# Kernel tuning notes

Hardware: AMD Instinct MI355X
Metric: run time of the kernel (lower is better)

The kernel has to match this reference:

```python
import jax, jax.numpy as jnp
import numpy as np
import math

N_HEAD = 16


def setup_inputs() -> dict:
    key = jax.random.key(0)
    ks = jax.random.split(key, 5)
    B, T, C = 2, 2048, 2048
    x = jax.random.normal(ks[0], (B, T, C), dtype=jnp.float32)
    # additive causal mask: 0 on/below diagonal, large negative above
    causal = jnp.tril(jnp.ones((T, T), dtype=bool))
    attention_mask = jnp.where(causal, 0.0, -1e9).astype(jnp.float32)[None, None]
    scale = 0.02
    W_attn = jax.random.normal(ks[1], (C, 3 * C), dtype=jnp.float32) * scale
    b_attn = jax.random.normal(ks[2], (3 * C,), dtype=jnp.float32) * scale
    W_proj = jax.random.normal(ks[3], (C, C), dtype=jnp.float32) * scale
    b_proj = jax.random.normal(ks[4], (C,), dtype=jnp.float32) * scale
    return {"x": x, "attention_mask": attention_mask, "W_attn": W_attn,
            "b_attn": b_attn, "W_proj": W_proj, "b_proj": b_proj}


def reference(x, attention_mask, W_attn, b_attn, W_proj, b_proj):
    B, T, C = x.shape
    H = N_HEAD
    Dh = C // H
    qkv = x @ W_attn + b_attn                      # [B,T,3C]
    q, k, v = jnp.split(qkv, 3, axis=2)            # each [B,T,C]
    current_cache = jnp.concatenate([k, v], axis=2)  # [B,T,2C]
    qh = q.reshape(B, T, H, Dh).transpose(0, 2, 1, 3)  # [B,H,T,Dh]
    kh = k.reshape(B, T, H, Dh).transpose(0, 2, 1, 3)
    vh = v.reshape(B, T, H, Dh).transpose(0, 2, 1, 3)
    att = jnp.einsum('bhqd,bhkd->bhqk', qh, kh) * (1.0 / math.sqrt(Dh))
    att = att + attention_mask                     # broadcast [1,1,T,T]
    att = jax.nn.softmax(att, axis=-1)
    y = jnp.einsum('bhqk,bhkd->bhqd', att, vh)     # [B,H,T,Dh]
    y = y.transpose(0, 2, 1, 3).reshape(B, T, C)
    y = y @ W_proj + b_proj                        # [B,T,C]
    return (y, current_cache)
```

## Files before the change

### kernel.cpp

```cpp
#include <hip/hip_runtime.h>

typedef __attribute__((ext_vector_type(8))) short bf16x8;
typedef __attribute__((ext_vector_type(4))) float f32x4;

#define MFMA16(a, b, c) __builtin_amdgcn_mfma_f32_16x16x32_bf16((a), (b), (c), 0, 0, 0)

static __device__ __forceinline__ short f2bf(float f) {
  unsigned u = __builtin_bit_cast(unsigned, f);
  unsigned r = (u + 0x7FFFu + ((u >> 16) & 1u)) >> 16;
  return (short)(unsigned short)r;
}
static __device__ __forceinline__ unsigned pack2(float lo, float hi) {
  return (unsigned)(unsigned short)f2bf(lo) | ((unsigned)(unsigned short)f2bf(hi) << 16);
}

static __device__ __forceinline__ void glds16(const void* g, void* l) {
  __builtin_amdgcn_global_load_lds((const __attribute__((address_space(1))) unsigned*)g,
                                   (__attribute__((address_space(3))) unsigned*)l, 16, 0, 0);
}

__global__ __launch_bounds__(256) void cvt_bf16_kernel(const float* __restrict__ in,
                                                       short* __restrict__ out) {
  size_t i = ((size_t)blockIdx.x * 256 + threadIdx.x) * 8;
  float4 a = *(const float4*)(in + i);
  float4 b = *(const float4*)(in + i + 4);
  uint4 o;
  o.x = pack2(a.x, a.y);
  o.y = pack2(a.z, a.w);
  o.z = pack2(b.x, b.y);
  o.w = pack2(b.z, b.w);
  *(uint4*)(out + i) = o;
}

__global__ __launch_bounds__(256) void transpose_cvt_kernel(const float* __restrict__ in,
                                                            short* __restrict__ out, int R,
                                                            int Cc) {
  __shared__ float tile[64][65];
  int tx = threadIdx.x & 15, ty = threadIdx.x >> 4;
  int r0 = blockIdx.y * 64, c0 = blockIdx.x * 64;
#pragma unroll
  for (int i = 0; i < 4; i++) {
    int r = ty + i * 16;
    float4 v = *(const float4*)(in + (size_t)(r0 + r) * Cc + c0 + tx * 4);
    tile[r][tx * 4 + 0] = v.x;
    tile[r][tx * 4 + 1] = v.y;
    tile[r][tx * 4 + 2] = v.z;
    tile[r][tx * 4 + 3] = v.w;
  }
  __syncthreads();
#pragma unroll
  for (int i = 0; i < 4; i++) {
    int co = ty + i * 16;
    uint2 o;
    o.x = pack2(tile[tx * 4 + 0][co], tile[tx * 4 + 1][co]);
    o.y = pack2(tile[tx * 4 + 2][co], tile[tx * 4 + 3][co]);
    *(uint2*)(out + (size_t)(c0 + co) * R + r0 + tx * 4) = o;
  }
}

__global__ __launch_bounds__(256) void gemm_qkv_kernel(const short* __restrict__ A,
                                                       const short* __restrict__ Bt,
                                                       const float* __restrict__ bias,
                                                       short* __restrict__ q_bf,
                                                       short* __restrict__ k_bf,
                                                       short* __restrict__ v_bf,
                                                       float* __restrict__ cache) {
  const int K = 2048;
  __shared__ __align__(16) short smem[128 * 64];
  short* As = smem;
  short* Bs = smem + 128 * 32;
  int tid = threadIdx.x;
  int lane = tid & 63, wid = tid >> 6;
  int wr = wid >> 1, wc = wid & 1;
  int l15 = lane & 15, l4 = lane >> 4;
  int rowBase = blockIdx.y * 128, colBase = blockIdx.x * 128;

  int srow = lane >> 2;
  int schunk = ((lane & 3) ^ ((lane >> 3) & 3)) * 8;
  int g0 = wid * 16, g1 = 64 + wid * 16;
  const short* Ag0 = A + (size_t)(rowBase + g0 + srow) * K + schunk;
  const short* Ag1 = A + (size_t)(rowBase + g1 + srow) * K + schunk;
  const short* Bg0 = Bt + (size_t)(colBase + g0 + srow) * K + schunk;
  const short* Bg1 = Bt + (size_t)(colBase + g1 + srow) * K + schunk;
  short* la0 = &As[g0 * 32];
  short* la1 = &As[g1 * 32];
  short* lb0 = &Bs[g0 * 32];
  short* lb1 = &Bs[g1 * 32];

  int fchunk = (l4 ^ ((l15 >> 1) & 3)) * 8;

  f32x4 zero = {0.f, 0.f, 0.f, 0.f};
  f32x4 acc[4][4];
#pragma unroll
  for (int i = 0; i < 4; i++)
#pragma unroll
    for (int j = 0; j < 4; j++) acc[i][j] = zero;

  for (int k0 = 0; k0 < K; k0 += 32) {
    __syncthreads();
    glds16(Ag0 + k0, la0);
    glds16(Ag1 + k0, la1);
    glds16(Bg0 + k0, lb0);
    glds16(Bg1 + k0, lb1);
    __syncthreads();
    bf16x8 af[4], bfv[4];
#pragma unroll
    for (int mt = 0; mt < 4; mt++)
      af[mt] = *(const bf16x8*)&As[(wr * 64 + mt * 16 + l15) * 32 + fchunk];
#pragma unroll
    for (int nt = 0; nt < 4; nt++)
      bfv[nt] = *(const bf16x8*)&Bs[(wc * 64 + nt * 16 + l15) * 32 + fchunk];
#pragma unroll
    for (int mt = 0; mt < 4; mt++)
#pragma unroll
      for (int nt = 0; nt < 4; nt++) acc[mt][nt] = MFMA16(af[mt], bfv[nt], acc[mt][nt]);
  }

  int seg = colBase >> 11;
  int colLoc = colBase & 2047;
  float scale = (seg == 0) ? 0.08838834764831845f : 1.0f;
  short* outp = (seg == 0) ? q_bf : (seg == 1) ? k_bf : v_bf;
  short(*Cs)[64] = (short(*)[64])smem;

  float bv[4];
#pragma unroll
  for (int nt = 0; nt < 4; nt++) bv[nt] = bias[colBase + wc * 64 + nt * 16 + l15];

#pragma unroll
  for (int p = 0; p < 2; p++) {
    __syncthreads();
    if (wc == p) {
#pragma unroll
      for (int mt = 0; mt < 4; mt++)
#pragma unroll
        for (int nt = 0; nt < 4; nt++)
#pragma unroll
          for (int r = 0; r < 4; r++)
            Cs[wr * 64 + mt * 16 + l4 * 4 + r][nt * 16 + l15] =
                f2bf((acc[mt][nt][r] + bv[nt]) * scale);
    }
    __syncthreads();
#pragma unroll
    for (int q = 0; q < 4; q++) {
      int row = q * 32 + (tid >> 3);
      int c8 = (tid & 7) * 8;
      *(uint4*)(outp + (size_t)(rowBase + row) * 2048 + colLoc + p * 64 + c8) =
          *(const uint4*)&Cs[row][c8];
    }
  }

  if (seg) {
    int coff = (seg == 1) ? 0 : 2048;
#pragma unroll
    for (int mt = 0; mt < 4; mt++)
#pragma unroll
      for (int nt = 0; nt < 4; nt++) {
        int cc = coff + colLoc + wc * 64 + nt * 16 + l15;
#pragma unroll
        for (int r = 0; r < 4; r++) {
          int row = rowBase + wr * 64 + mt * 16 + l4 * 4 + r;
          cache[(size_t)row * 4096 + cc] = acc[mt][nt][r] + bv[nt];
        }
      }
  }
}

__global__ __launch_bounds__(256) void vpost_kernel(const short* __restrict__ vb,
                                                    short* __restrict__ vt) {
  __shared__ short tile[64][72];
  int tid = threadIdx.x;
  int z = blockIdx.z;
  int b = z >> 4, hh = z & 15;
  int t0 = blockIdx.x * 64, d0 = blockIdx.y * 64;
  int tx = tid & 7, ty = tid >> 3;
#pragma unroll
  for (int i = 0; i < 2; i++) {
    int r = ty + i * 32;
    *(uint4*)&tile[r][tx * 8] =
        *(const uint4*)(vb + (size_t)(b * 2048 + t0 + r) * 2048 + hh * 128 + d0 + tx * 8);
  }
  __syncthreads();
#pragma unroll
  for (int i = 0; i < 2; i++) {
    int dr = ty + i * 32;
    short tmp[8];
#pragma unroll
    for (int j = 0; j < 8; j++) {
      int p = tx * 8 + j;
      int tl = (p & 32) + ((p & 1) << 4) + ((p >> 1) & 15);
      tmp[j] = tile[tl][dr];
    }
    *(uint4*)(vt + (size_t)(z * 128 + d0 + dr) * 2048 + t0 + tx * 8) = *(uint4*)tmp;
  }
}

__global__ __launch_bounds__(256) void gemm_proj_kernel(const short* __restrict__ A,
                                                        const short* __restrict__ Bt,
                                                        const float* __restrict__ bias,
                                                        float* __restrict__ out_y) {
  const int K = 2048;
  __shared__ __align__(16) short As[128 * 32];
  __shared__ __align__(16) short Bs[128 * 32];
  int tid = threadIdx.x;
  int lane = tid & 63, wid = tid >> 6;
  int wr = wid >> 1, wc = wid & 1;
  int l15 = lane & 15, l4 = lane >> 4;
  int rowBase = blockIdx.y * 128, colBase = blockIdx.x * 128;

  int srow = lane >> 2;
  int schunk = ((lane & 3) ^ ((lane >> 3) & 3)) * 8;
  int g0 = wid * 16, g1 = 64 + wid * 16;
  const short* Ag0 = A + (size_t)(rowBase + g0 + srow) * K + schunk;
  const short* Ag1 = A + (size_t)(rowBase + g1 + srow) * K + schunk;
  const short* Bg0 = Bt + (size_t)(colBase + g0 + srow) * K + schunk;
  const short* Bg1 = Bt + (size_t)(colBase + g1 + srow) * K + schunk;
  short* la0 = &As[g0 * 32];
  short* la1 = &As[g1 * 32];
  short* lb0 = &Bs[g0 * 32];
  short* lb1 = &Bs[g1 * 32];

  int fchunk = (l4 ^ ((l15 >> 1) & 3)) * 8;

  f32x4 zero = {0.f, 0.f, 0.f, 0.f};
  f32x4 acc[4][4];
#pragma unroll
  for (int i = 0; i < 4; i++)
#pragma unroll
    for (int j = 0; j < 4; j++) acc[i][j] = zero;

  for (int k0 = 0; k0 < K; k0 += 32) {
    __syncthreads();
    glds16(Ag0 + k0, la0);
    glds16(Ag1 + k0, la1);
    glds16(Bg0 + k0, lb0);
    glds16(Bg1 + k0, lb1);
    __syncthreads();
    bf16x8 af[4], bfv[4];
#pragma unroll
    for (int mt = 0; mt < 4; mt++)
      af[mt] = *(const bf16x8*)&As[(wr * 64 + mt * 16 + l15) * 32 + fchunk];
#pragma unroll
    for (int nt = 0; nt < 4; nt++)
      bfv[nt] = *(const bf16x8*)&Bs[(wc * 64 + nt * 16 + l15) * 32 + fchunk];
#pragma unroll
    for (int mt = 0; mt < 4; mt++)
#pragma unroll
      for (int nt = 0; nt < 4; nt++) acc[mt][nt] = MFMA16(af[mt], bfv[nt], acc[mt][nt]);
  }

#pragma unroll
  for (int mt = 0; mt < 4; mt++) {
#pragma unroll
    for (int nt = 0; nt < 4; nt++) {
      int col = colBase + wc * 64 + nt * 16 + l15;
      float bvv = bias[col];
#pragma unroll
      for (int r = 0; r < 4; r++) {
        int row = rowBase + wr * 64 + mt * 16 + l4 * 4 + r;
        out_y[(size_t)row * 2048 + col] = acc[mt][nt][r] + bvv;
      }
    }
  }
}

#define LDK 136
#define LDV 72
#define LDP 72

__global__ __launch_bounds__(512, 4) void attn_kernel(const short* __restrict__ qb,
                                                      const short* __restrict__ kb,
                                                      const short* __restrict__ vtb,
                                                      short* __restrict__ attout) {
  __shared__ short Ks[64 * LDK];
  __shared__ short Vs[128 * LDV];
  __shared__ short Ps[8][16 * LDP];

  int tid = threadIdx.x;
  int lane = tid & 63, wid = tid >> 6;
  int l15 = lane & 15, l4 = lane >> 4;
  int qlo = blockIdx.x, qhi = 31 - qlo;
  int h = blockIdx.y, b = blockIdx.z;
  int myqt = (wid < 4) ? qhi : qlo;
  int qrow0 = myqt * 64 + (wid & 3) * 16;
  size_t qkbase = (size_t)b * 2048 * 2048 + (size_t)h * 128;
  size_t vbase = (size_t)((b * 16 + h) * 128) * 2048;

  bf16x8 qf[4];
#pragma unroll
  for (int kk = 0; kk < 4; kk++)
    qf[kk] = *(const bf16x8*)(qb + qkbase + (size_t)(qrow0 + l15) * 2048 + kk * 32 + l4 * 8);

  short onev = (short)0x3F80;
  bf16x8 ones = {onev, onev, onev, onev, onev, onev, onev, onev};

  f32x4 zero = {0.f, 0.f, 0.f, 0.f};
  f32x4 o[8], ol;
#pragma unroll
  for (int n = 0; n < 8; n++) o[n] = zero;
  ol = zero;

  for (int kt = 0; kt <= qhi; kt++) {
    int kt0 = kt * 64;
    __syncthreads();
#pragma unroll
    for (int i = 0; i < 2; i++) {
      int c = i * 512 + tid;
      int kr = c >> 4, kc = (c & 15) * 8;
      *(uint4*)&Ks[kr * LDK + kc] = *(const uint4*)(kb + qkbase + (size_t)(kt0 + kr) * 2048 + kc);
    }
#pragma unroll
    for (int i = 0; i < 2; i++) {
      int c = i * 512 + tid;
      int dr = c >> 3, tc = (c & 7) * 8;
      *(uint4*)&Vs[dr * LDV + tc] = *(const uint4*)(vtb + vbase + (size_t)dr * 2048 + kt0 + tc);
    }
    __syncthreads();

    if (wid < 4 || kt <= qlo) {
      f32x4 s[4];
#pragma unroll
      for (int nt = 0; nt < 4; nt++) s[nt] = zero;
#pragma unroll
      for (int kk = 0; kk < 4; kk++) {
#pragma unroll
        for (int nt = 0; nt < 4; nt++) {
          bf16x8 kf = *(const bf16x8*)&Ks[(nt * 16 + l15) * LDK + kk * 32 + l4 * 8];
          s[nt] = MFMA16(qf[kk], kf, s[nt]);
        }
      }

      if (kt == myqt) {
#pragma unroll
        for (int nt = 0; nt < 4; nt++) {
          int colg = kt0 + nt * 16 + l15;
#pragma unroll
          for (int r = 0; r < 4; r++) {
            int rowg = qrow0 + l4 * 4 + r;
            if (colg > rowg) s[nt][r] = -1e30f;
          }
        }
      }

#pragma unroll
      for (int r = 0; r < 4; r++) {
        float p0 = __expf(s[0][r]);
        float p1 = __expf(s[1][r]);
        float p2 = __expf(s[2][r]);
        float p3 = __expf(s[3][r]);
        int prow = (l4 * 4 + r) * LDP;
        *(unsigned*)&Ps[wid][prow + 2 * l15] = pack2(p0, p1);
        *(unsigned*)&Ps[wid][prow + 32 + 2 * l15] = pack2(p2, p3);
      }

#pragma unroll
      for (int kk = 0; kk < 2; kk++) {
        bf16x8 pf = *(const bf16x8*)&Ps[wid][l15 * LDP + kk * 32 + l4 * 8];
        ol = MFMA16(pf, ones, ol);
#pragma unroll
        for (int n = 0; n < 8; n++) {
          bf16x8 vf = *(const bf16x8*)&Vs[(n * 16 + l15) * LDV + kk * 32 + l4 * 8];
          o[n] = MFMA16(pf, vf, o[n]);
        }
      }
    }
  }

  float rl[4];
#pragma unroll
  for (int r = 0; r < 4; r++) rl[r] = 1.0f / ol[r];
#pragma unroll
  for (int n = 0; n < 8; n++)
#pragma unroll
    for (int r = 0; r < 4; r++)
      attout[qkbase + (size_t)(qrow0 + l4 * 4 + r) * 2048 + n * 16 + l15] =
          f2bf(o[n][r] * rl[r]);
}

extern "C" void kernel_launch(void* const* d_in, const int* in_sizes, int n_in, void* d_out,
                              int out_size, void* d_ws, size_t ws_size, hipStream_t stream) {
  const float* x = (const float*)d_in[0];
  const float* W_attn = (const float*)d_in[2];
  const float* b_attn = (const float*)d_in[3];
  const float* W_proj = (const float*)d_in[4];
  const float* b_proj = (const float*)d_in[5];
  float* y = (float*)d_out;
  float* cache = y + (size_t)4096 * 2048;

  char* p = (char*)d_ws;
  short* x_bf = (short*)p;   p += (size_t)8388608 * 2;
  short* q_bf = (short*)p;   p += (size_t)8388608 * 2;
  short* k_bf = (short*)p;   p += (size_t)8388608 * 2;
  short* vt_bf = (short*)p;  p += (size_t)8388608 * 2;
  short* att_bf = (short*)p; p += (size_t)8388608 * 2;
  short* wt_attn = (short*)p; p += (size_t)12582912 * 2;
  short* wt_proj = (short*)p; p += (size_t)4194304 * 2;
  short* v_bf = att_bf;

  cvt_bf16_kernel<<<4096, 256, 0, stream>>>(x, x_bf);
  transpose_cvt_kernel<<<dim3(96, 32), 256, 0, stream>>>(W_attn, wt_attn, 2048, 6144);
  transpose_cvt_kernel<<<dim3(32, 32), 256, 0, stream>>>(W_proj, wt_proj, 2048, 2048);
  gemm_qkv_kernel<<<dim3(48, 32), 256, 0, stream>>>(x_bf, wt_attn, b_attn, q_bf, k_bf, v_bf,
                                                    cache);
  vpost_kernel<<<dim3(32, 2, 32), 256, 0, stream>>>(v_bf, vt_bf);
  attn_kernel<<<dim3(16, 16, 2), 512, 0, stream>>>(q_bf, k_bf, vt_bf, att_bf);
  gemm_proj_kernel<<<dim3(16, 32), 256, 0, stream>>>(att_bf, wt_proj, b_proj, y);
}
```

Before: 460.2 us.

## Rewrite QKV GEMM as 256x256 tiles with double-buffered LDS pipelining

```diff
diff --git a/kernel.cpp b/kernel.cpp
--- a/kernel.cpp
+++ b/kernel.cpp
@@ -58,93 +58,170 @@
   }
 }
 
-__global__ __launch_bounds__(256) void gemm_qkv_kernel(const short* __restrict__ A,
-                                                       const short* __restrict__ Bt,
-                                                       const float* __restrict__ bias,
-                                                       short* __restrict__ q_bf,
-                                                       short* __restrict__ k_bf,
-                                                       short* __restrict__ v_bf,
-                                                       float* __restrict__ cache) {
-  const int K = 2048;
-  __shared__ __align__(16) short smem[128 * 64];
-  short* As = smem;
-  short* Bs = smem + 128 * 32;
+
+#define AF(C, KS, MT) (*(const bf16x8*)&lds[(C)*32768 + (KS)*8192 + (wr8 + (MT)) * 512 + rdoff])
+#define BF_(C, KS, NT) \
+  (*(const bf16x8*)&lds[(C)*32768 + 16384 + (KS)*8192 + (wc4 + (NT)) * 512 + rdoff])
+
+#define STAGE_A(C, KS, KT)                                                      \
+  do {                                                                          \
+    glds16(Asrc0 + (KT) * 64 + (KS) * 32, &lds[(C)*32768 + (KS)*8192 + wid * 512]); \
+    glds16(Asrc1 + (KT) * 64 + (KS) * 32,                                       \
+           &lds[(C)*32768 + (KS)*8192 + (wid + 8) * 512]);                      \
+  } while (0)
+#define STAGE_B(C, KS, KT)                                                      \
+  do {                                                                          \
+    glds16(Bsrc0 + (KT) * 64 + (KS) * 32,                                       \
+           &lds[(C)*32768 + 16384 + (KS)*8192 + wid * 512]);                    \
+    glds16(Bsrc1 + (KT) * 64 + (KS) * 32,                                       \
+           &lds[(C)*32768 + 16384 + (KS)*8192 + (wid + 8) * 512]);              \
+  } while (0)
+
+#define MIDBAR                                                       \
+  do {                                                               \
+    asm volatile("s_barrier\n\ts_waitcnt lgkmcnt(0)" ::: "memory");  \
+    __builtin_amdgcn_sched_barrier(0);                               \
+  } while (0)
+#define ENDBAR                                       \
+  do {                                               \
+    __builtin_amdgcn_sched_barrier(0);               \
+    asm volatile("s_barrier" ::: "memory");          \
+    __builtin_amdgcn_sched_barrier(0);               \
+  } while (0)
+#define ENDBARV                                                      \
+  do {                                                               \
+    __builtin_amdgcn_sched_barrier(0);                               \
+    asm volatile("s_waitcnt vmcnt(8)\n\ts_barrier" ::: "memory");    \
+    __builtin_amdgcn_sched_barrier(0);                               \
+  } while (0)
+
+#define MMROW(AR, MT)                          \
+  do {                                         \
+    acc[MT][0] = MFMA16(AR, bfr[0], acc[MT][0]); \
+    acc[MT][1] = MFMA16(AR, bfr[1], acc[MT][1]); \
+    acc[MT][2] = MFMA16(AR, bfr[2], acc[MT][2]); \
+    acc[MT][3] = MFMA16(AR, bfr[3], acc[MT][3]); \
+  } while (0)
+
+#define PHASE(C, KS, MB, STG, WAITV)                                         \
+  do {                                                                       \
+    af[0] = AF(C, KS, MB + 0);                                               \
+    af[1] = AF(C, KS, MB + 1);                                               \
+    af[2] = AF(C, KS, MB + 2);                                               \
+    af[3] = AF(C, KS, MB + 3);                                               \
+    if ((MB) == 0) {                                                         \
+      bfr[0] = BF_(C, KS, 0);                                                \
+      bfr[1] = BF_(C, KS, 1);                                                \
+      bfr[2] = BF_(C, KS, 2);                                                \
+      bfr[3] = BF_(C, KS, 3);                                                \
+    }                                                                        \
+    STG;                                                                     \
+    MIDBAR;                                                                  \
+    __builtin_amdgcn_s_setprio(1);                                           \
+    MMROW(af[0], MB + 0);                                                    \
+    MMROW(af[1], MB + 1);                                                    \
+    MMROW(af[2], MB + 2);                                                    \
+    MMROW(af[3], MB + 3);                                                    \
+    __builtin_amdgcn_s_setprio(0);                                           \
+    if (WAITV) { ENDBARV; } else { ENDBAR; }                                 \
+  } while (0)
+
+#define KTILE(C, NX, MM)                       \
+  do {                                         \
+    int s23 = (MM) + 1 > 31 ? 31 : (MM) + 1;   \
+    int s01 = (MM) + 2 > 31 ? 31 : (MM) + 2;   \
+    PHASE(C, 0, 0, STAGE_A(NX, 1, s23), 0);    \
+    PHASE(C, 0, 4, STAGE_B(NX, 1, s23), 1);    \
+    PHASE(C, 1, 0, STAGE_A(C, 0, s01), 0);     \
+    PHASE(C, 1, 4, STAGE_B(C, 0, s01), 1);     \
+  } while (0)
+
+__global__ __launch_bounds__(512, 2) void gemm_qkv_kernel(const short* __restrict__ A,
+                                                          const short* __restrict__ Bt,
+                                                          const float* __restrict__ bias,
+                                                          short* __restrict__ q_bf,
+                                                          short* __restrict__ k_bf,
+                                                          short* __restrict__ v_bf,
+                                                          float* __restrict__ cache) {
+  __shared__ __align__(16) short lds[65536];
   int tid = threadIdx.x;
   int lane = tid & 63, wid = tid >> 6;
-  int wr = wid >> 1, wc = wid & 1;
   int l15 = lane & 15, l4 = lane >> 4;
-  int rowBase = blockIdx.y * 128, colBase = blockIdx.x * 128;
-
-  int srow = lane >> 2;
-  int schunk = ((lane & 3) ^ ((lane >> 3) & 3)) * 8;
-  int g0 = wid * 16, g1 = 64 + wid * 16;
-  const short* Ag0 = A + (size_t)(rowBase + g0 + srow) * K + schunk;
-  const short* Ag1 = A + (size_t)(rowBase + g1 + srow) * K + schunk;
-  const short* Bg0 = Bt + (size_t)(colBase + g0 + srow) * K + schunk;
-  const short* Bg1 = Bt + (size_t)(colBase + g1 + srow) * K + schunk;
-  short* la0 = &As[g0 * 32];
-  short* la1 = &As[g1 * 32];
-  short* lb0 = &Bs[g0 * 32];
-  short* lb1 = &Bs[g1 * 32];
-
-  int fchunk = (l4 ^ ((l15 >> 1) & 3)) * 8;
+  int wr = wid >> 2, wc = wid & 3;
+  int wr8 = wr * 8, wc4 = wc * 4;
+
+  int bid = blockIdx.x;
+  int s = (bid & 7) * 48 + (bid >> 3);
+  int bx = s % 24, by = s / 24;
+  int rowBase = by * 256, colBase = bx * 256;
+
+  int wprime = (lane * 16) ^ (lane & 32);
+  int r_ = wprime >> 6;
+  int cs_ = (wprime & 63) >> 1;
+  const short* Asrc0 = A + (size_t)(rowBase + wid * 16 + r_) * 2048 + cs_;
+  const short* Asrc1 = A + (size_t)(rowBase + (wid + 8) * 16 + r_) * 2048 + cs_;
+  const short* Bsrc0 = Bt + (size_t)(colBase + wid * 16 + r_) * 2048 + cs_;
+  const short* Bsrc1 = Bt + (size_t)(colBase + (wid + 8) * 16 + r_) * 2048 + cs_;
+
+  int rdoff = l15 * 32 + ((l4 * 8) ^ ((l15 & 8) << 1));
 
   f32x4 zero = {0.f, 0.f, 0.f, 0.f};
-  f32x4 acc[4][4];
-#pragma unroll
-  for (int i = 0; i < 4; i++)
+  f32x4 acc[8][4];
+#pragma unroll
+  for (int i = 0; i < 8; i++)
 #pragma unroll
     for (int j = 0; j < 4; j++) acc[i][j] = zero;
 
-  for (int k0 = 0; k0 < K; k0 += 32) {
-    __syncthreads();
-    glds16(Ag0 + k0, la0);
-    glds16(Ag1 + k0, la1);
-    glds16(Bg0 + k0, lb0);
-    glds16(Bg1 + k0, lb1);
-    __syncthreads();
-    bf16x8 af[4], bfv[4];
-#pragma unroll
-    for (int mt = 0; mt < 4; mt++)
-      af[mt] = *(const bf16x8*)&As[(wr * 64 + mt * 16 + l15) * 32 + fchunk];
-#pragma unroll
-    for (int nt = 0; nt < 4; nt++)
-      bfv[nt] = *(const bf16x8*)&Bs[(wc * 64 + nt * 16 + l15) * 32 + fchunk];
-#pragma unroll
-    for (int mt = 0; mt < 4; mt++)
-#pragma unroll
-      for (int nt = 0; nt < 4; nt++) acc[mt][nt] = MFMA16(af[mt], bfv[nt], acc[mt][nt]);
-  }
+  bf16x8 af[4], bfr[4];
+
+  STAGE_A(0, 0, 0);
+  STAGE_B(0, 0, 0);
+  STAGE_A(0, 1, 0);
+  STAGE_B(0, 1, 0);
+  STAGE_A(1, 0, 1);
+  STAGE_B(1, 0, 1);
+  asm volatile("s_waitcnt vmcnt(8)" ::: "memory");
+  __builtin_amdgcn_sched_barrier(0);
+  asm volatile("s_barrier" ::: "memory");
+  __builtin_amdgcn_sched_barrier(0);
+
+  for (int it = 0; it < 16; ++it) {
+    int m0 = it * 2;
+    KTILE(0, 1, m0);
+    KTILE(1, 0, m0 + 1);
+  }
+
+  asm volatile("s_waitcnt vmcnt(0)" ::: "memory");
+  __syncthreads();
 
   int seg = colBase >> 11;
   int colLoc = colBase & 2047;
   float scale = (seg == 0) ? 0.08838834764831845f : 1.0f;
   short* outp = (seg == 0) ? q_bf : (seg == 1) ? k_bf : v_bf;
-  short(*Cs)[64] = (short(*)[64])smem;
-
   float bv[4];
 #pragma unroll
   for (int nt = 0; nt < 4; nt++) bv[nt] = bias[colBase + wc * 64 + nt * 16 + l15];
 
-#pragma unroll
-  for (int p = 0; p < 2; p++) {
+  short(*Cs)[264] = (short(*)[264])lds;
+#pragma unroll
+  for (int half = 0; half < 2; half++) {
+    if (half) __syncthreads();
+    if (wr == half) {
+#pragma unroll
+      for (int mt = 0; mt < 8; mt++)
+#pragma unroll
+        for (int nt = 0; nt < 4; nt++)
+#pragma unroll
+          for (int r = 0; r < 4; r++)
+            Cs[mt * 16 + l4 * 4 + r][wc * 64 + nt * 16 + l15] =
+                f2bf((acc[mt][nt][r] + bv[nt]) * scale);
+    }
     __syncthreads();
-    if (wc == p) {
-#pragma unroll
-      for (int mt = 0; mt < 4; mt++)
-#pragma unroll
-        for (int nt = 0; nt < 4; nt++)
-#pragma unroll
-          for (int r = 0; r < 4; r++)
-            Cs[wr * 64 + mt * 16 + l4 * 4 + r][nt * 16 + l15] =
-                f2bf((acc[mt][nt][r] + bv[nt]) * scale);
-    }
-    __syncthreads();
-#pragma unroll
-    for (int q = 0; q < 4; q++) {
-      int row = q * 32 + (tid >> 3);
-      int c8 = (tid & 7) * 8;
-      *(uint4*)(outp + (size_t)(rowBase + row) * 2048 + colLoc + p * 64 + c8) =
+#pragma unroll
+    for (int pp = 0; pp < 8; pp++) {
+      int row = pp * 16 + (tid >> 5);
+      int c8 = (tid & 31) * 8;
+      *(uint4*)(outp + (size_t)(rowBase + half * 128 + row) * 2048 + colLoc + c8) =
           *(const uint4*)&Cs[row][c8];
     }
   }
@@ -152,13 +229,13 @@
   if (seg) {
     int coff = (seg == 1) ? 0 : 2048;
 #pragma unroll
-    for (int mt = 0; mt < 4; mt++)
+    for (int mt = 0; mt < 8; mt++)
 #pragma unroll
       for (int nt = 0; nt < 4; nt++) {
         int cc = coff + colLoc + wc * 64 + nt * 16 + l15;
 #pragma unroll
         for (int r = 0; r < 4; r++) {
-          int row = rowBase + wr * 64 + mt * 16 + l4 * 4 + r;
+          int row = rowBase + wr * 128 + mt * 16 + l4 * 4 + r;
           cache[(size_t)row * 4096 + cc] = acc[mt][nt][r] + bv[nt];
         }
       }
@@ -399,8 +476,7 @@
   cvt_bf16_kernel<<<4096, 256, 0, stream>>>(x, x_bf);
   transpose_cvt_kernel<<<dim3(96, 32), 256, 0, stream>>>(W_attn, wt_attn, 2048, 6144);
   transpose_cvt_kernel<<<dim3(32, 32), 256, 0, stream>>>(W_proj, wt_proj, 2048, 2048);
-  gemm_qkv_kernel<<<dim3(48, 32), 256, 0, stream>>>(x_bf, wt_attn, b_attn, q_bf, k_bf, v_bf,
-                                                    cache);
+  gemm_qkv_kernel<<<384, 512, 0, stream>>>(x_bf, wt_attn, b_attn, q_bf, k_bf, v_bf, cache);
   vpost_kernel<<<dim3(32, 2, 32), 256, 0, stream>>>(v_bf, vt_bf);
   attn_kernel<<<dim3(16, 16, 2), 512, 0, stream>>>(q_bf, k_bf, vt_bf, att_bf);
   gemm_proj_kernel<<<dim3(16, 32), 256, 0, stream>>>(att_bf, wt_proj, b_proj, y);
```

After: 437.1 us. 5.0% less time.

## Rewrite QKV and projection GEMMs with pipelined 256x128 tiles and XCD-aware block mapping

Applied to the files above, without the earlier changes.

```diff
diff --git a/kernel.cpp b/kernel.cpp
--- a/kernel.cpp
+++ b/kernel.cpp
@@ -58,95 +58,141 @@
   }
 }
 
-__global__ __launch_bounds__(256) void gemm_qkv_kernel(const short* __restrict__ A,
-                                                       const short* __restrict__ Bt,
-                                                       const float* __restrict__ bias,
-                                                       short* __restrict__ q_bf,
-                                                       short* __restrict__ k_bf,
-                                                       short* __restrict__ v_bf,
-                                                       float* __restrict__ cache) {
-  const int K = 2048;
-  __shared__ __align__(16) short smem[128 * 64];
-  short* As = smem;
-  short* Bs = smem + 128 * 32;
-  int tid = threadIdx.x;
-  int lane = tid & 63, wid = tid >> 6;
-  int wr = wid >> 1, wc = wid & 1;
-  int l15 = lane & 15, l4 = lane >> 4;
-  int rowBase = blockIdx.y * 128, colBase = blockIdx.x * 128;
-
-  int srow = lane >> 2;
-  int schunk = ((lane & 3) ^ ((lane >> 3) & 3)) * 8;
-  int g0 = wid * 16, g1 = 64 + wid * 16;
-  const short* Ag0 = A + (size_t)(rowBase + g0 + srow) * K + schunk;
-  const short* Ag1 = A + (size_t)(rowBase + g1 + srow) * K + schunk;
-  const short* Bg0 = Bt + (size_t)(colBase + g0 + srow) * K + schunk;
-  const short* Bg1 = Bt + (size_t)(colBase + g1 + srow) * K + schunk;
-  short* la0 = &As[g0 * 32];
-  short* la1 = &As[g1 * 32];
-  short* lb0 = &Bs[g0 * 32];
-  short* lb1 = &Bs[g1 * 32];
-
-  int fchunk = (l4 ^ ((l15 >> 1) & 3)) * 8;
-
-  f32x4 zero = {0.f, 0.f, 0.f, 0.f};
-  f32x4 acc[4][4];
-#pragma unroll
-  for (int i = 0; i < 4; i++)
-#pragma unroll
-    for (int j = 0; j < 4; j++) acc[i][j] = zero;
-
-  for (int k0 = 0; k0 < K; k0 += 32) {
-    __syncthreads();
-    glds16(Ag0 + k0, la0);
-    glds16(Ag1 + k0, la1);
-    glds16(Bg0 + k0, lb0);
-    glds16(Bg1 + k0, lb1);
-    __syncthreads();
-    bf16x8 af[4], bfv[4];
-#pragma unroll
-    for (int mt = 0; mt < 4; mt++)
-      af[mt] = *(const bf16x8*)&As[(wr * 64 + mt * 16 + l15) * 32 + fchunk];
-#pragma unroll
-    for (int nt = 0; nt < 4; nt++)
-      bfv[nt] = *(const bf16x8*)&Bs[(wc * 64 + nt * 16 + l15) * 32 + fchunk];
-#pragma unroll
-    for (int mt = 0; mt < 4; mt++)
-#pragma unroll
-      for (int nt = 0; nt < 4; nt++) acc[mt][nt] = MFMA16(af[mt], bfv[nt], acc[mt][nt]);
-  }
+
+#define AFQ(C, KS, MT) (*(const bf16x8*)&lds[(C)*16384 + (KS)*8192 + (wr4 + (MT)) * 512 + rdoff])
+#define BFQ(C, KS, NT) \
+  (*(const bf16x8*)&lds[32768 + (C)*8192 + (KS)*4096 + (wc4 + (NT)) * 512 + rdoff])
+
+#define STAGE(C, KS, KT)                                                           \
+  do {                                                                             \
+    glds16(Asrc0 + (KT) * 64 + (KS) * 32, &lds[(C)*16384 + (KS)*8192 + wid * 512]); \
+    glds16(Asrc1 + (KT) * 64 + (KS) * 32,                                          \
+           &lds[(C)*16384 + (KS)*8192 + (wid + 8) * 512]);                         \
+    glds16(Bsrc0 + (KT) * 64 + (KS) * 32,                                          \
+           &lds[32768 + (C)*8192 + (KS)*4096 + wid * 512]);                        \
+  } while (0)
+
+#define MIDBAR                                                       \
+  do {                                                               \
+    asm volatile("s_barrier\n\ts_waitcnt lgkmcnt(0)" ::: "memory");  \
+    __builtin_amdgcn_sched_barrier(0);                               \
+  } while (0)
+#define ENDBARV6                                                     \
+  do {                                                               \
+    __builtin_amdgcn_sched_barrier(0);                               \
+    asm volatile("s_waitcnt vmcnt(6)\n\ts_barrier" ::: "memory");    \
+    __builtin_amdgcn_sched_barrier(0);                               \
+  } while (0)
+
+#define MMROW(AR, MT)                            \
+  do {                                           \
+    acc[MT][0] = MFMA16(AR, bfr[0], acc[MT][0]); \
+    acc[MT][1] = MFMA16(AR, bfr[1], acc[MT][1]); \
+    acc[MT][2] = MFMA16(AR, bfr[2], acc[MT][2]); \
+    acc[MT][3] = MFMA16(AR, bfr[3], acc[MT][3]); \
+  } while (0)
+
+#define PHASE(C, KS, STG)          \
+  do {                             \
+    af[0] = AFQ(C, KS, 0);         \
+    af[1] = AFQ(C, KS, 1);         \
+    af[2] = AFQ(C, KS, 2);         \
+    af[3] = AFQ(C, KS, 3);         \
+    bfr[0] = BFQ(C, KS, 0);        \
+    bfr[1] = BFQ(C, KS, 1);        \
+    bfr[2] = BFQ(C, KS, 2);        \
+    bfr[3] = BFQ(C, KS, 3);        \
+    STG;                           \
+    MIDBAR;                        \
+    __builtin_amdgcn_s_setprio(1); \
+    MMROW(af[0], 0);               \
+    MMROW(af[1], 1);               \
+    MMROW(af[2], 2);               \
+    MMROW(af[3], 3);               \
+    __builtin_amdgcn_s_setprio(0); \
+    ENDBARV6;                      \
+  } while (0)
+
+#define KTILE(C, NX, MM)                     \
+  do {                                       \
+    int s1 = (MM) + 1 > 31 ? 31 : (MM) + 1;  \
+    int s2 = (MM) + 2 > 31 ? 31 : (MM) + 2;  \
+    PHASE(C, 0, STAGE(NX, 1, s1));           \
+    PHASE(C, 1, STAGE(C, 0, s2));            \
+  } while (0)
+
+#define GEMM_PREAMBLE(Aptr, Bptr)                                                  \
+  __shared__ __align__(16) short lds[49152];                           \
+  int tid = threadIdx.x;                                                           \
+  int lane = tid & 63, wid = tid >> 6;                                             \
+  int l15 = lane & 15, l4 = lane >> 4;                                             \
+  int wr = wid >> 1, wc = wid & 1;                                                 \
+  int wr4 = wr * 4, wc4 = wc * 4;                                                  \
+  int wprime = (lane * 16) ^ (lane & 32);                                          \
+  int r_ = wprime >> 6;                                                            \
+  int cs_ = (wprime & 63) >> 1;                                                    \
+  const short* Asrc0 = (Aptr) + (size_t)(rowBase + wid * 16 + r_) * 2048 + cs_;    \
+  const short* Asrc1 = (Aptr) + (size_t)(rowBase + (wid + 8) * 16 + r_) * 2048 + cs_; \
+  const short* Bsrc0 = (Bptr) + (size_t)(colBase + wid * 16 + r_) * 2048 + cs_;    \
+  int rdoff = l15 * 32 + ((l4 * 8) ^ ((l15 & 8) << 1));                            \
+  f32x4 zero = {0.f, 0.f, 0.f, 0.f};                                               \
+  f32x4 acc[4][4];                                                                 \
+  _Pragma("unroll") for (int i = 0; i < 4; i++) _Pragma("unroll") for (int j = 0;  \
+                                                                       j < 4; j++) \
+      acc[i][j] = zero;                                                            \
+  bf16x8 af[4], bfr[4];                                                            \
+  STAGE(0, 0, 0);                                                                  \
+  STAGE(0, 1, 0);                                                                  \
+  STAGE(1, 0, 1);                                                                  \
+  asm volatile("s_waitcnt vmcnt(6)" ::: "memory");                                 \
+  __builtin_amdgcn_sched_barrier(0);                                               \
+  asm volatile("s_barrier" ::: "memory");                                          \
+  __builtin_amdgcn_sched_barrier(0);                                               \
+  for (int it = 0; it < 16; ++it) {                                                \
+    int m0 = it * 2;                                                               \
+    KTILE(0, 1, m0);                                                               \
+    KTILE(1, 0, m0 + 1);                                                           \
+  }                                                                                \
+  asm volatile("s_waitcnt vmcnt(0)" ::: "memory");                                 \
+  __syncthreads();
+
+__global__ __launch_bounds__(512, 2) void gemm_qkv_kernel(const short* __restrict__ A,
+                                                          const short* __restrict__ Bt,
+                                                          const float* __restrict__ bias,
+                                                          short* __restrict__ q_bf,
+                                                          short* __restrict__ k_bf,
+                                                          short* __restrict__ v_bf,
+                                                          float* __restrict__ cache) {
+  int bid = blockIdx.x;
+  int s = (bid & 7) * 96 + (bid >> 3);
+  int bx = s % 48, by = s / 48;
+  int rowBase = by * 256, colBase = bx * 128;
+
+  GEMM_PREAMBLE(A, Bt)
 
   int seg = colBase >> 11;
   int colLoc = colBase & 2047;
   float scale = (seg == 0) ? 0.08838834764831845f : 1.0f;
   short* outp = (seg == 0) ? q_bf : (seg == 1) ? k_bf : v_bf;
-  short(*Cs)[64] = (short(*)[64])smem;
-
   float bv[4];
 #pragma unroll
   for (int nt = 0; nt < 4; nt++) bv[nt] = bias[colBase + wc * 64 + nt * 16 + l15];
 
-#pragma unroll
-  for (int p = 0; p < 2; p++) {
-    __syncthreads();
-    if (wc == p) {
-#pragma unroll
-      for (int mt = 0; mt < 4; mt++)
-#pragma unroll
-        for (int nt = 0; nt < 4; nt++)
-#pragma unroll
-          for (int r = 0; r < 4; r++)
-            Cs[wr * 64 + mt * 16 + l4 * 4 + r][nt * 16 + l15] =
-                f2bf((acc[mt][nt][r] + bv[nt]) * scale);
-    }
-    __syncthreads();
-#pragma unroll
-    for (int q = 0; q < 4; q++) {
-      int row = q * 32 + (tid >> 3);
-      int c8 = (tid & 7) * 8;
-      *(uint4*)(outp + (size_t)(rowBase + row) * 2048 + colLoc + p * 64 + c8) =
-          *(const uint4*)&Cs[row][c8];
-    }
+  short(*Cs)[136] = (short(*)[136])lds;
+#pragma unroll
+  for (int mt = 0; mt < 4; mt++)
+#pragma unroll
+    for (int nt = 0; nt < 4; nt++)
+#pragma unroll
+      for (int r = 0; r < 4; r++)
+        Cs[wr * 64 + mt * 16 + l4 * 4 + r][wc * 64 + nt * 16 + l15] =
+            f2bf((acc[mt][nt][r] + bv[nt]) * scale);
+  __syncthreads();
+#pragma unroll
+  for (int pp = 0; pp < 8; pp++) {
+    int idx = pp * 512 + tid;
+    int row = idx >> 4, c8 = (idx & 15) * 8;
+    *(uint4*)(outp + (size_t)(rowBase + row) * 2048 + colLoc + c8) = *(const uint4*)&Cs[row][c8];
   }
 
   if (seg) {
@@ -163,6 +209,31 @@
         }
       }
   }
+}
+
+__global__ __launch_bounds__(512, 2) void gemm_proj_kernel(const short* __restrict__ A,
+                                                           const short* __restrict__ Bt,
+                                                           const float* __restrict__ bias,
+                                                           float* __restrict__ out_y) {
+  int bid = blockIdx.x;
+  int s = (bid & 7) * 32 + (bid >> 3);
+  int bx = s % 16, by = s / 16;
+  int rowBase = by * 256, colBase = bx * 128;
+
+  GEMM_PREAMBLE(A, Bt)
+
+#pragma unroll
+  for (int mt = 0; mt < 4; mt++)
+#pragma unroll
+    for (int nt = 0; nt < 4; nt++) {
+      int col = colBase + wc * 64 + nt * 16 + l15;
+      float bvv = bias[col];
+#pragma unroll
+      for (int r = 0; r < 4; r++) {
+        int row = rowBase + wr * 64 + mt * 16 + l4 * 4 + r;
+        out_y[(size_t)row * 2048 + col] = acc[mt][nt][r] + bvv;
+      }
+    }
 }
 
 __global__ __launch_bounds__(256) void vpost_kernel(const short* __restrict__ vb,
@@ -191,75 +262,6 @@
       tmp[j] = tile[tl][dr];
     }
     *(uint4*)(vt + (size_t)(z * 128 + d0 + dr) * 2048 + t0 + tx * 8) = *(uint4*)tmp;
-  }
-}
-
-__global__ __launch_bounds__(256) void gemm_proj_kernel(const short* __restrict__ A,
-                                                        const short* __restrict__ Bt,
-                                                        const float* __restrict__ bias,
-                                                        float* __restrict__ out_y) {
-  const int K = 2048;
-  __shared__ __align__(16) short As[128 * 32];
-  __shared__ __align__(16) short Bs[128 * 32];
-  int tid = threadIdx.x;
-  int lane = tid & 63, wid = tid >> 6;
-  int wr = wid >> 1, wc = wid & 1;
-  int l15 = lane & 15, l4 = lane >> 4;
-  int rowBase = blockIdx.y * 128, colBase = blockIdx.x * 128;
-
-  int srow = lane >> 2;
-  int schunk = ((lane & 3) ^ ((lane >> 3) & 3)) * 8;
-  int g0 = wid * 16, g1 = 64 + wid * 16;
-  const short* Ag0 = A + (size_t)(rowBase + g0 + srow) * K + schunk;
-  const short* Ag1 = A + (size_t)(rowBase + g1 + srow) * K + schunk;
-  const short* Bg0 = Bt + (size_t)(colBase + g0 + srow) * K + schunk;
-  const short* Bg1 = Bt + (size_t)(colBase + g1 + srow) * K + schunk;
-  short* la0 = &As[g0 * 32];
-  short* la1 = &As[g1 * 32];
-  short* lb0 = &Bs[g0 * 32];
-  short* lb1 = &Bs[g1 * 32];
-
-  int fchunk = (l4 ^ ((l15 >> 1) & 3)) * 8;
-
-  f32x4 zero = {0.f, 0.f, 0.f, 0.f};
-  f32x4 acc[4][4];
-#pragma unroll
-  for (int i = 0; i < 4; i++)
-#pragma unroll
-    for (int j = 0; j < 4; j++) acc[i][j] = zero;
-
-  for (int k0 = 0; k0 < K; k0 += 32) {
-    __syncthreads();
-    glds16(Ag0 + k0, la0);
-    glds16(Ag1 + k0, la1);
-    glds16(Bg0 + k0, lb0);
-    glds16(Bg1 + k0, lb1);
-    __syncthreads();
-    bf16x8 af[4], bfv[4];
-#pragma unroll
-    for (int mt = 0; mt < 4; mt++)
-      af[mt] = *(const bf16x8*)&As[(wr * 64 + mt * 16 + l15) * 32 + fchunk];
-#pragma unroll
-    for (int nt = 0; nt < 4; nt++)
-      bfv[nt] = *(const bf16x8*)&Bs[(wc * 64 + nt * 16 + l15) * 32 + fchunk];
-#pragma unroll
-    for (int mt = 0; mt < 4; mt++)
-#pragma unroll
-      for (int nt = 0; nt < 4; nt++) acc[mt][nt] = MFMA16(af[mt], bfv[nt], acc[mt][nt]);
-  }
-
-#pragma unroll
-  for (int mt = 0; mt < 4; mt++) {
-#pragma unroll
-    for (int nt = 0; nt < 4; nt++) {
-      int col = colBase + wc * 64 + nt * 16 + l15;
-      float bvv = bias[col];
-#pragma unroll
-      for (int r = 0; r < 4; r++) {
-        int row = rowBase + wr * 64 + mt * 16 + l4 * 4 + r;
-        out_y[(size_t)row * 2048 + col] = acc[mt][nt][r] + bvv;
-      }
-    }
   }
 }
 
@@ -399,9 +401,8 @@
   cvt_bf16_kernel<<<4096, 256, 0, stream>>>(x, x_bf);
   transpose_cvt_kernel<<<dim3(96, 32), 256, 0, stream>>>(W_attn, wt_attn, 2048, 6144);
   transpose_cvt_kernel<<<dim3(32, 32), 256, 0, stream>>>(W_proj, wt_proj, 2048, 2048);
-  gemm_qkv_kernel<<<dim3(48, 32), 256, 0, stream>>>(x_bf, wt_attn, b_attn, q_bf, k_bf, v_bf,
-                                                    cache);
+  gemm_qkv_kernel<<<768, 512, 0, stream>>>(x_bf, wt_attn, b_attn, q_bf, k_bf, v_bf, cache);
   vpost_kernel<<<dim3(32, 2, 32), 256, 0, stream>>>(v_bf, vt_bf);
   attn_kernel<<<dim3(16, 16, 2), 512, 0, stream>>>(q_bf, k_bf, vt_bf, att_bf);
-  gemm_proj_kernel<<<dim3(16, 32), 256, 0, stream>>>(att_bf, wt_proj, b_proj, y);
-}
+  gemm_proj_kernel<<<256, 512, 0, stream>>>(att_bf, wt_proj, b_proj, y);
+}
```

Result: faster. 432.5 us (-6.0%).
